# Kernel optimization log

Measured on AMD Instinct MI355X. Metric: run time of the kernel, lower is better.

The kernel has to match this reference:

```python
import jax, jax.numpy as jnp
import numpy as np

DIMS = [14400, 7200, 3600, 1800, 900, 450]  # in_dim then floor(dim/2) per layer
K = 25
BATCH = 256
NSTEPS = 10
OUT_DIM = 2


def setup_inputs() -> dict:
    key = jax.random.key(0)
    ks = jax.random.split(key, 13)
    inp = {"input": jax.random.normal(ks[0], (BATCH, NSTEPS, DIMS[0]), dtype=jnp.float32)}
    w_scale = (2.0 / K) ** 0.5  # matches normal_(0, (2/K)**0.5) init
    for i in range(5):
        d_prev, d = DIMS[i], DIMS[i + 1]
        inp[f"knn{i}"] = jax.random.randint(ks[1 + i], (d, K), 0, d_prev)
        inp[f"w{i}"] = w_scale * jax.random.normal(ks[6 + i], (d, K), dtype=jnp.float32)
        inp[f"b{i}"] = jnp.zeros((1, d), dtype=jnp.float32)
    inp["fc_w"] = jax.random.normal(ks[11], (OUT_DIM, DIMS[-1]), dtype=jnp.float32) * (1.0 / DIMS[-1] ** 0.5)
    inp["fc_b"] = jnp.zeros((OUT_DIM,), dtype=jnp.float32)
    return inp


def reference(input, knn0, knn1, knn2, knn3, knn4,
              w0, w1, w2, w3, w4, b0, b1, b2, b3, b4, fc_w, fc_b):
    # Faithful to the torch module: the synapses/membranes dicts are never
    # reassigned inside the step loop, so every snntorch Synaptic call sees
    # zero state: reset = Heaviside(0 - thr) = 0, syn = alpha*0 + I = I,
    # mem = beta*0 + syn = I.  The returned mem (x) is therefore exactly the
    # layer drive, there is no cross-step recurrence, and `angles` is
    # overwritten each step, so only the final timestep reaches the output.
    knns = (knn0, knn1, knn2, knn3, knn4)
    ws = (w0, w1, w2, w3, w4)
    bs = (b0, b1, b2, b3, b4)
    x = input[:, -1, :]  # [B, in_dim] -- last step (permute(1,0,2) then input[step])
    for knn, w, b in zip(knns, ws, bs):
        # gather KNN inputs [B, dim, K], weight locally, reduce over K, add bias
        x = jnp.einsum('bdk,dk->bd', x[:, knn], w) + b
    angles = x @ fc_w.T + fc_b  # fc_angle
    return angles  # (mem4_rec, spk4_rec are empty lists in the original)
```

## Files before the change

kernel.cpp:

```cpp
#include <hip/hip_runtime.h>

#define NSTEPS 10
#define D_IN   14400
#define BATCH  256
#define KNN_K  25

#define L0D 7200
#define L1D 3600
#define L2D 1800
#define L3D 900
#define L4D 450

#define G0 113
#define G1 57
#define G2 29
#define G3 15
#define G4 8
#define SPG 832
#define O0 0
#define O1 (G0*SPG)
#define O2 (O1 + G1*SPG)
#define O3 (O2 + G2*SPG)
#define O4 (O3 + G3*SPG)
#define OTOT (O4 + G4*SPG)

__device__ __forceinline__ unsigned bf16b(float x) {
    unsigned u = __float_as_uint(x);
    return (u + 0x7fffu + ((u >> 16) & 1u)) >> 16;
}

__device__ __forceinline__ void gpair(unsigned u, const char* actb, float& s0, float& s1) {
    unsigned av = *(const unsigned*)(actb + (u & 0xffffu));
    float wf = __uint_as_float(u & 0xffff0000u);
    s0 = fmaf(__uint_as_float(av << 16),          wf, s0);
    s1 = fmaf(__uint_as_float(av & 0xffff0000u),  wf, s1);
}

__global__ void repack_tiles(const int* __restrict__ k0, const float* __restrict__ w0,
                             const int* __restrict__ k1, const float* __restrict__ w1,
                             const int* __restrict__ k2, const float* __restrict__ w2,
                             const int* __restrict__ k3, const float* __restrict__ w3,
                             const int* __restrict__ k4, const float* __restrict__ w4,
                             uint2* __restrict__ tile)
{
    int s = blockIdx.x * 256 + threadIdx.x;
    if (s >= OTOT) return;
    const int* kp; const float* wp; int dim, t;
    if      (s < O1) { kp = k0; wp = w0; dim = L0D; t = s;      }
    else if (s < O2) { kp = k1; wp = w1; dim = L1D; t = s - O1; }
    else if (s < O3) { kp = k2; wp = w2; dim = L2D; t = s - O2; }
    else if (s < O4) { kp = k3; wp = w3; dim = L3D; t = s - O3; }
    else             { kp = k4; wp = w4; dim = L4D; t = s - O4; }
    int g    = t / SPG;
    int rem  = t - g * SPG;
    int j    = rem >> 6;
    int lane = rem & 63;
    int r    = g * 64 + lane;
    unsigned vx = 0, vy = 0;
    if (r < dim) {
        int e0 = 2 * j, e1 = 2 * j + 1;
        if (e0 < KNN_K) vx = (bf16b(wp[r * KNN_K + e0]) << 16) | ((unsigned)kp[r * KNN_K + e0] << 2);
        if (e1 < KNN_K) vy = (bf16b(wp[r * KNN_K + e1]) << 16) | ((unsigned)kp[r * KNN_K + e1] << 2);
    }
    tile[s] = make_uint2(vx, vy);
}

__global__ __launch_bounds__(512, 4)
void lcn_l0(const float* __restrict__ input, const uint2* __restrict__ tile,
            const float* __restrict__ bias0, unsigned* __restrict__ y0)
{
    __shared__ unsigned act[D_IN];
    const int tid = threadIdx.x;
    const int p   = blockIdx.x & 127;
    const int h   = blockIdx.x >> 7;

    const float4* r0 = (const float4*)(input + ((size_t)(2 * p)     * NSTEPS + (NSTEPS - 1)) * D_IN);
    const float4* r1 = (const float4*)(input + ((size_t)(2 * p + 1) * NSTEPS + (NSTEPS - 1)) * D_IN);
    for (int i = tid; i < D_IN / 4; i += 512) {
        float4 a = r0[i], b = r1[i];
        uint4 wd;
        wd.x = bf16b(a.x) | (bf16b(b.x) << 16);
        wd.y = bf16b(a.y) | (bf16b(b.y) << 16);
        wd.z = bf16b(a.z) | (bf16b(b.z) << 16);
        wd.w = bf16b(a.w) | (bf16b(b.w) << 16);
        *(uint4*)(act + i * 4) = wd;
    }
    __syncthreads();
    const char* actb = (const char*)act;

    const int rbase = h ? 3584 : 0;
    const int rend  = h ? 7200 : 3584;
#pragma unroll
    for (int i = 0; i < 8; ++i) {
        int r = rbase + tid + i * 512;
        if (r < rend) {
            const uint2* tp = tile + (size_t)(r >> 6) * SPG + (r & 63);
            float s0 = bias0[r], s1 = s0;
#pragma unroll
            for (int j = 0; j < 13; ++j) {
                uint2 u = tp[j * 64];
                gpair(u.x, actb, s0, s1);
                gpair(u.y, actb, s0, s1);
            }
            y0[(size_t)p * L0D + r] = bf16b(s0) | (bf16b(s1) << 16);
        }
    }
}

template<int DIM>
__device__ __forceinline__ void k2_layer(unsigned* act, const uint2* tile,
                                         const float* __restrict__ bias, int tid)
{
    constexpr int NI = (DIM + 1023) / 1024;
    float s0[NI], s1[NI];
    const char* actb = (const char*)act;
#pragma unroll
    for (int i = 0; i < NI; ++i) {
        int r = tid + i * 1024;
        if (r < DIM) {
            const uint2* tp = tile + (size_t)(r >> 6) * SPG + (r & 63);
            float a = bias[r], b = a;
#pragma unroll
            for (int j = 0; j < 13; ++j) {
                uint2 u = tp[j * 64];
                gpair(u.x, actb, a, b);
                gpair(u.y, actb, a, b);
            }
            s0[i] = a; s1[i] = b;
        }
    }
    __syncthreads();
#pragma unroll
    for (int i = 0; i < NI; ++i) {
        int r = tid + i * 1024;
        if (r < DIM) act[r] = bf16b(s0[i]) | (bf16b(s1[i]) << 16);
    }
    __syncthreads();
}

__global__ __launch_bounds__(1024, 4)
void lcn_rest(const unsigned* __restrict__ y0, const uint2* __restrict__ tile,
              const float* __restrict__ bias1, const float* __restrict__ bias2,
              const float* __restrict__ bias3, const float* __restrict__ bias4,
              const float* __restrict__ fc_w,  const float* __restrict__ fc_b,
              float* __restrict__ out)
{
    __shared__ unsigned act[L0D];
    const int tid = threadIdx.x;
    const int p   = blockIdx.x;

    const uint4* src = (const uint4*)(y0 + (size_t)p * L0D);
#pragma unroll
    for (int i = 0; i < 2; ++i) {
        int q = tid + i * 1024;
        if (q < L0D / 4) *(uint4*)(act + q * 4) = src[q];
    }
    __syncthreads();

    k2_layer<L1D>(act, tile + O1, bias1, tid);
    k2_layer<L2D>(act, tile + O2, bias2, tid);
    k2_layer<L3D>(act, tile + O3, bias3, tid);
    k2_layer<L4D>(act, tile + O4, bias4, tid);

    const int wv = tid >> 6, lane = tid & 63;
    if (wv < 4) {
        const int j = wv & 1, o = wv >> 1;
        float s = 0.f;
#pragma unroll
        for (int it = 0; it < 8; ++it) {
            int r = lane + it * 64;
            if (r < L4D) {
                unsigned av = act[r];
                float xv = j ? __uint_as_float(av & 0xffff0000u)
                             : __uint_as_float(av << 16);
                s += xv * fc_w[o * L4D + r];
            }
        }
#pragma unroll
        for (int off = 32; off > 0; off >>= 1) s += __shfl_xor(s, off);
        if (lane == 0) out[(2 * p + j) * 2 + o] = s + fc_b[o];
    }
}

extern "C" void kernel_launch(void* const* d_in, const int* in_sizes, int n_in,
                              void* d_out, int out_size, void* d_ws, size_t ws_size,
                              hipStream_t stream) {
    const float* input = (const float*)d_in[0];
    const int*   knn[5];
    const float* w[5];
    const float* bias[5];
    for (int i = 0; i < 5; ++i) {
        knn[i]  = (const int*)  d_in[1 + 3 * i];
        w[i]    = (const float*)d_in[2 + 3 * i];
        bias[i] = (const float*)d_in[3 + 3 * i];
    }
    const float* fc_w = (const float*)d_in[16];
    const float* fc_b = (const float*)d_in[17];
    float* out = (float*)d_out;

    uint2*    tile = (uint2*)d_ws;
    unsigned* y0   = (unsigned*)((char*)d_ws + (size_t)OTOT * 8);

    repack_tiles<<<(OTOT + 255) / 256, 256, 0, stream>>>(
        knn[0], w[0], knn[1], w[1], knn[2], w[2], knn[3], w[3], knn[4], w[4], tile);

    lcn_l0<<<256, 512, 0, stream>>>(input, tile, bias[0], y0);

    lcn_rest<<<128, 1024, 0, stream>>>(y0, tile, bias[1], bias[2], bias[3], bias[4],
                                       fc_w, fc_b, out);
}
```

Baseline: 37.45 us.

## Split layer 1 into its own two-way-split kernel and pre-pack input in prep

Moves the fp32-to-bf16 packing of the last-timestep input into the prep kernel, so layer 0 blocks only copy already-packed pairs into shared memory. Layer 1 is pulled out of the single-block-per-pair tail kernel into a separate kernel with 256 blocks, each computing half the rows, which doubles parallelism for that layer. The layer 0 launch bound changes from 4 to 2 blocks per CU. The cost is an extra kernel launch and extra global round trips for the packed input and the layer-1 output.

```diff
diff --git a/kernel.cpp b/kernel.cpp
--- a/kernel.cpp
+++ b/kernel.cpp
@@ -17,13 +17,15 @@
 #define G3 15
 #define G4 8
 #define SPG 832
-#define O0 0
 #define O1 (G0*SPG)
 #define O2 (O1 + G1*SPG)
 #define O3 (O2 + G2*SPG)
 #define O4 (O3 + G3*SPG)
 #define OTOT (O4 + G4*SPG)
 
+#define NPAIR 128
+#define NPACK (NPAIR * (D_IN/4))
+
 __device__ __forceinline__ unsigned bf16b(float x) {
     unsigned u = __float_as_uint(x);
     return (u + 0x7fffu + ((u >> 16) & 1u)) >> 16;
@@ -36,55 +38,63 @@
     s1 = fmaf(__uint_as_float(av & 0xffff0000u),  wf, s1);
 }
 
-__global__ void repack_tiles(const int* __restrict__ k0, const float* __restrict__ w0,
-                             const int* __restrict__ k1, const float* __restrict__ w1,
-                             const int* __restrict__ k2, const float* __restrict__ w2,
-                             const int* __restrict__ k3, const float* __restrict__ w3,
-                             const int* __restrict__ k4, const float* __restrict__ w4,
-                             uint2* __restrict__ tile)
+__global__ void prep_kernel(const int* __restrict__ k0, const float* __restrict__ w0,
+                            const int* __restrict__ k1, const float* __restrict__ w1,
+                            const int* __restrict__ k2, const float* __restrict__ w2,
+                            const int* __restrict__ k3, const float* __restrict__ w3,
+                            const int* __restrict__ k4, const float* __restrict__ w4,
+                            const float* __restrict__ input,
+                            uint2* __restrict__ tile, uint4* __restrict__ xpk)
 {
     int s = blockIdx.x * 256 + threadIdx.x;
-    if (s >= OTOT) return;
-    const int* kp; const float* wp; int dim, t;
-    if      (s < O1) { kp = k0; wp = w0; dim = L0D; t = s;      }
-    else if (s < O2) { kp = k1; wp = w1; dim = L1D; t = s - O1; }
-    else if (s < O3) { kp = k2; wp = w2; dim = L2D; t = s - O2; }
-    else if (s < O4) { kp = k3; wp = w3; dim = L3D; t = s - O3; }
-    else             { kp = k4; wp = w4; dim = L4D; t = s - O4; }
-    int g    = t / SPG;
-    int rem  = t - g * SPG;
-    int j    = rem >> 6;
-    int lane = rem & 63;
-    int r    = g * 64 + lane;
-    unsigned vx = 0, vy = 0;
-    if (r < dim) {
-        int e0 = 2 * j, e1 = 2 * j + 1;
-        if (e0 < KNN_K) vx = (bf16b(wp[r * KNN_K + e0]) << 16) | ((unsigned)kp[r * KNN_K + e0] << 2);
-        if (e1 < KNN_K) vy = (bf16b(wp[r * KNN_K + e1]) << 16) | ((unsigned)kp[r * KNN_K + e1] << 2);
-    }
-    tile[s] = make_uint2(vx, vy);
-}
-
-__global__ __launch_bounds__(512, 4)
-void lcn_l0(const float* __restrict__ input, const uint2* __restrict__ tile,
-            const float* __restrict__ bias0, unsigned* __restrict__ y0)
-{
-    __shared__ unsigned act[D_IN];
-    const int tid = threadIdx.x;
-    const int p   = blockIdx.x & 127;
-    const int h   = blockIdx.x >> 7;
-
-    const float4* r0 = (const float4*)(input + ((size_t)(2 * p)     * NSTEPS + (NSTEPS - 1)) * D_IN);
-    const float4* r1 = (const float4*)(input + ((size_t)(2 * p + 1) * NSTEPS + (NSTEPS - 1)) * D_IN);
-    for (int i = tid; i < D_IN / 4; i += 512) {
-        float4 a = r0[i], b = r1[i];
+    if (s < OTOT) {
+        const int* kp; const float* wp; int dim, t;
+        if      (s < O1) { kp = k0; wp = w0; dim = L0D; t = s;      }
+        else if (s < O2) { kp = k1; wp = w1; dim = L1D; t = s - O1; }
+        else if (s < O3) { kp = k2; wp = w2; dim = L2D; t = s - O2; }
+        else if (s < O4) { kp = k3; wp = w3; dim = L3D; t = s - O3; }
+        else             { kp = k4; wp = w4; dim = L4D; t = s - O4; }
+        int g    = t / SPG;
+        int rem  = t - g * SPG;
+        int j    = rem >> 6;
+        int lane = rem & 63;
+        int r    = g * 64 + lane;
+        unsigned vx = 0, vy = 0;
+        if (r < dim) {
+            int e0 = 2 * j, e1 = 2 * j + 1;
+            if (e0 < KNN_K) vx = (bf16b(wp[r * KNN_K + e0]) << 16) | ((unsigned)kp[r * KNN_K + e0] << 2);
+            if (e1 < KNN_K) vy = (bf16b(wp[r * KNN_K + e1]) << 16) | ((unsigned)kp[r * KNN_K + e1] << 2);
+        }
+        tile[s] = make_uint2(vx, vy);
+        return;
+    }
+    int t = s - OTOT;
+    if (t < NPACK) {
+        int p = t / (D_IN / 4);
+        int c = t - p * (D_IN / 4);
+        const float4 a = *(const float4*)(input + ((size_t)(2 * p)     * NSTEPS + (NSTEPS - 1)) * D_IN + 4 * c);
+        const float4 b = *(const float4*)(input + ((size_t)(2 * p + 1) * NSTEPS + (NSTEPS - 1)) * D_IN + 4 * c);
         uint4 wd;
         wd.x = bf16b(a.x) | (bf16b(b.x) << 16);
         wd.y = bf16b(a.y) | (bf16b(b.y) << 16);
         wd.z = bf16b(a.z) | (bf16b(b.z) << 16);
         wd.w = bf16b(a.w) | (bf16b(b.w) << 16);
-        *(uint4*)(act + i * 4) = wd;
-    }
+        xpk[(size_t)p * (D_IN / 4) + c] = wd;
+    }
+}
+
+__global__ __launch_bounds__(512, 2)
+void lcn_l0(const uint4* __restrict__ xpk, const uint2* __restrict__ tile,
+            const float* __restrict__ bias0, unsigned* __restrict__ y0)
+{
+    __shared__ unsigned act[D_IN];
+    const int tid = threadIdx.x;
+    const int p   = blockIdx.x & 127;
+    const int h   = blockIdx.x >> 7;
+
+    const uint4* src = xpk + (size_t)p * (D_IN / 4);
+    for (int i = tid; i < D_IN / 4; i += 512)
+        *(uint4*)(act + i * 4) = src[i];
     __syncthreads();
     const char* actb = (const char*)act;
 
@@ -107,6 +117,40 @@
     }
 }
 
+__global__ __launch_bounds__(512, 4)
+void lcn_l1(const unsigned* __restrict__ y0, const uint2* __restrict__ tile,
+            const float* __restrict__ bias1, unsigned* __restrict__ y1)
+{
+    __shared__ unsigned act[L0D];
+    const int tid = threadIdx.x;
+    const int p   = blockIdx.x & 127;
+    const int h   = blockIdx.x >> 7;
+
+    const uint4* src = (const uint4*)(y0 + (size_t)p * L0D);
+    for (int i = tid; i < L0D / 4; i += 512)
+        *(uint4*)(act + i * 4) = src[i];
+    __syncthreads();
+    const char* actb = (const char*)act;
+
+    const int rbase = h ? 1792 : 0;
+    const int rend  = h ? 3600 : 1792;
+#pragma unroll
+    for (int i = 0; i < 4; ++i) {
+        int r = rbase + tid + i * 512;
+        if (r < rend) {
+            const uint2* tp = tile + O1 + (size_t)(r >> 6) * SPG + (r & 63);
+            float s0 = bias1[r], s1 = s0;
+#pragma unroll
+            for (int j = 0; j < 13; ++j) {
+                uint2 u = tp[j * 64];
+                gpair(u.x, actb, s0, s1);
+                gpair(u.y, actb, s0, s1);
+            }
+            y1[(size_t)p * L1D + r] = bf16b(s0) | (bf16b(s1) << 16);
+        }
+    }
+}
+
 template<int DIM>
 __device__ __forceinline__ void k2_layer(unsigned* act, const uint2* tile,
                                          const float* __restrict__ bias, int tid)
@@ -139,25 +183,20 @@
 }
 
 __global__ __launch_bounds__(1024, 4)
-void lcn_rest(const unsigned* __restrict__ y0, const uint2* __restrict__ tile,
-              const float* __restrict__ bias1, const float* __restrict__ bias2,
-              const float* __restrict__ bias3, const float* __restrict__ bias4,
+void lcn_rest(const unsigned* __restrict__ y1, const uint2* __restrict__ tile,
+              const float* __restrict__ bias2, const float* __restrict__ bias3,
+              const float* __restrict__ bias4,
               const float* __restrict__ fc_w,  const float* __restrict__ fc_b,
               float* __restrict__ out)
 {
-    __shared__ unsigned act[L0D];
+    __shared__ unsigned act[L1D];
     const int tid = threadIdx.x;
     const int p   = blockIdx.x;
 
-    const uint4* src = (const uint4*)(y0 + (size_t)p * L0D);
-#pragma unroll
-    for (int i = 0; i < 2; ++i) {
-        int q = tid + i * 1024;
-        if (q < L0D / 4) *(uint4*)(act + q * 4) = src[q];
-    }
-    __syncthreads();
-
-    k2_layer<L1D>(act, tile + O1, bias1, tid);
+    const uint4* src = (const uint4*)(y1 + (size_t)p * L1D);
+    if (tid < L1D / 4) *(uint4*)(act + tid * 4) = src[tid];
+    __syncthreads();
+
     k2_layer<L2D>(act, tile + O2, bias2, tid);
     k2_layer<L3D>(act, tile + O3, bias3, tid);
     k2_layer<L4D>(act, tile + O4, bias4, tid);
@@ -198,14 +237,20 @@
     const float* fc_b = (const float*)d_in[17];
     float* out = (float*)d_out;
 
-    uint2*    tile = (uint2*)d_ws;
-    unsigned* y0   = (unsigned*)((char*)d_ws + (size_t)OTOT * 8);
-
-    repack_tiles<<<(OTOT + 255) / 256, 256, 0, stream>>>(
-        knn[0], w[0], knn[1], w[1], knn[2], w[2], knn[3], w[3], knn[4], w[4], tile);
-
-    lcn_l0<<<256, 512, 0, stream>>>(input, tile, bias[0], y0);
-
-    lcn_rest<<<128, 1024, 0, stream>>>(y0, tile, bias[1], bias[2], bias[3], bias[4],
+    char* base = (char*)d_ws;
+    uint2*    tile = (uint2*)   base;
+    uint4*    xpk  = (uint4*)  (base + (size_t)OTOT * 8);
+    unsigned* y0   = (unsigned*)(base + (size_t)OTOT * 8 + (size_t)NPAIR * D_IN * 4);
+    unsigned* y1   = (unsigned*)(base + (size_t)OTOT * 8 + (size_t)NPAIR * D_IN * 4
+                                      + (size_t)NPAIR * L0D * 4);
+
+    const int nprep = OTOT + NPACK;
+    prep_kernel<<<(nprep + 255) / 256, 256, 0, stream>>>(
+        knn[0], w[0], knn[1], w[1], knn[2], w[2], knn[3], w[3], knn[4], w[4],
+        input, tile, xpk);
+
+    lcn_l0<<<256, 512, 0, stream>>>(xpk, tile, bias[0], y0);
+    lcn_l1<<<256, 512, 0, stream>>>(y0, tile, bias[1], y1);
+    lcn_rest<<<128, 1024, 0, stream>>>(y1, tile, bias[2], bias[3], bias[4],
                                        fc_w, fc_b, out);
 }
```

Result: no change. 37.16 us (-0.8%).

## Pack four batch rows per gather and split layers across more kernels

Applied to the files above, without the earlier changes.

Activations are now packed as four bf16 batch rows per 8-byte LDS word, so each gathered neighbor index feeds four FMAs instead of two. This halves the number of KNN gathers and tile reads per sample. The input bf16 packing moves into the prep kernel alongside the weight repack. Layers 0-2 each become a separate kernel that splits rows four ways across blocks, giving 256 blocks per layer instead of 128 serial blocks for the later layers. The cost is more kernel launches and extra global round trips for the y1 and y2 intermediates, and a 115KB LDS buffer in layer 0 that limits it to one block per CU.

```diff
diff --git a/kernel.cpp b/kernel.cpp
--- a/kernel.cpp
+++ b/kernel.cpp
@@ -2,7 +2,6 @@
 
 #define NSTEPS 10
 #define D_IN   14400
-#define BATCH  256
 #define KNN_K  25
 
 #define L0D 7200
@@ -17,168 +16,222 @@
 #define G3 15
 #define G4 8
 #define SPG 832
-#define O0 0
 #define O1 (G0*SPG)
 #define O2 (O1 + G1*SPG)
 #define O3 (O2 + G2*SPG)
 #define O4 (O3 + G3*SPG)
 #define OTOT (O4 + G4*SPG)
 
+#define NG    64
+#define PACKQ (D_IN/4)
+#define NPACK (NG * PACKQ)
+
 __device__ __forceinline__ unsigned bf16b(float x) {
     unsigned u = __float_as_uint(x);
     return (u + 0x7fffu + ((u >> 16) & 1u)) >> 16;
 }
 
-__device__ __forceinline__ void gpair(unsigned u, const char* actb, float& s0, float& s1) {
-    unsigned av = *(const unsigned*)(actb + (u & 0xffffu));
-    float wf = __uint_as_float(u & 0xffff0000u);
-    s0 = fmaf(__uint_as_float(av << 16),          wf, s0);
-    s1 = fmaf(__uint_as_float(av & 0xffff0000u),  wf, s1);
-}
-
-__global__ void repack_tiles(const int* __restrict__ k0, const float* __restrict__ w0,
-                             const int* __restrict__ k1, const float* __restrict__ w1,
-                             const int* __restrict__ k2, const float* __restrict__ w2,
-                             const int* __restrict__ k3, const float* __restrict__ w3,
-                             const int* __restrict__ k4, const float* __restrict__ w4,
-                             uint2* __restrict__ tile)
+__device__ __forceinline__ void gp4(unsigned u, const char* actb,
+                                    float& a0, float& a1, float& a2, float& a3) {
+    const uint2 av = *(const uint2*)(actb + 8u * (u & 0xffffu));
+    const float wf = __uint_as_float(u & 0xffff0000u);
+    a0 = fmaf(__uint_as_float(av.x << 16),         wf, a0);
+    a1 = fmaf(__uint_as_float(av.x & 0xffff0000u), wf, a1);
+    a2 = fmaf(__uint_as_float(av.y << 16),         wf, a2);
+    a3 = fmaf(__uint_as_float(av.y & 0xffff0000u), wf, a3);
+}
+
+__global__ void prep_kernel(const int* __restrict__ k0, const float* __restrict__ w0,
+                            const int* __restrict__ k1, const float* __restrict__ w1,
+                            const int* __restrict__ k2, const float* __restrict__ w2,
+                            const int* __restrict__ k3, const float* __restrict__ w3,
+                            const int* __restrict__ k4, const float* __restrict__ w4,
+                            const float* __restrict__ input,
+                            uint2* __restrict__ tile, uint2* __restrict__ xpk)
 {
     int s = blockIdx.x * 256 + threadIdx.x;
-    if (s >= OTOT) return;
-    const int* kp; const float* wp; int dim, t;
-    if      (s < O1) { kp = k0; wp = w0; dim = L0D; t = s;      }
-    else if (s < O2) { kp = k1; wp = w1; dim = L1D; t = s - O1; }
-    else if (s < O3) { kp = k2; wp = w2; dim = L2D; t = s - O2; }
-    else if (s < O4) { kp = k3; wp = w3; dim = L3D; t = s - O3; }
-    else             { kp = k4; wp = w4; dim = L4D; t = s - O4; }
-    int g    = t / SPG;
-    int rem  = t - g * SPG;
-    int j    = rem >> 6;
-    int lane = rem & 63;
-    int r    = g * 64 + lane;
-    unsigned vx = 0, vy = 0;
-    if (r < dim) {
-        int e0 = 2 * j, e1 = 2 * j + 1;
-        if (e0 < KNN_K) vx = (bf16b(wp[r * KNN_K + e0]) << 16) | ((unsigned)kp[r * KNN_K + e0] << 2);
-        if (e1 < KNN_K) vy = (bf16b(wp[r * KNN_K + e1]) << 16) | ((unsigned)kp[r * KNN_K + e1] << 2);
-    }
-    tile[s] = make_uint2(vx, vy);
-}
-
-__global__ __launch_bounds__(512, 4)
-void lcn_l0(const float* __restrict__ input, const uint2* __restrict__ tile,
-            const float* __restrict__ bias0, unsigned* __restrict__ y0)
-{
-    __shared__ unsigned act[D_IN];
-    const int tid = threadIdx.x;
-    const int p   = blockIdx.x & 127;
-    const int h   = blockIdx.x >> 7;
-
-    const float4* r0 = (const float4*)(input + ((size_t)(2 * p)     * NSTEPS + (NSTEPS - 1)) * D_IN);
-    const float4* r1 = (const float4*)(input + ((size_t)(2 * p + 1) * NSTEPS + (NSTEPS - 1)) * D_IN);
-    for (int i = tid; i < D_IN / 4; i += 512) {
-        float4 a = r0[i], b = r1[i];
-        uint4 wd;
-        wd.x = bf16b(a.x) | (bf16b(b.x) << 16);
-        wd.y = bf16b(a.y) | (bf16b(b.y) << 16);
-        wd.z = bf16b(a.z) | (bf16b(b.z) << 16);
-        wd.w = bf16b(a.w) | (bf16b(b.w) << 16);
-        *(uint4*)(act + i * 4) = wd;
-    }
+    if (s < OTOT) {
+        const int* kp; const float* wp; int dim, t;
+        if      (s < O1) { kp = k0; wp = w0; dim = L0D; t = s;      }
+        else if (s < O2) { kp = k1; wp = w1; dim = L1D; t = s - O1; }
+        else if (s < O3) { kp = k2; wp = w2; dim = L2D; t = s - O2; }
+        else if (s < O4) { kp = k3; wp = w3; dim = L3D; t = s - O3; }
+        else             { kp = k4; wp = w4; dim = L4D; t = s - O4; }
+        int g    = t / SPG;
+        int rem  = t - g * SPG;
+        int j    = rem >> 6;
+        int lane = rem & 63;
+        int r    = g * 64 + lane;
+        unsigned vx = 0, vy = 0;
+        if (r < dim) {
+            int e0 = 2 * j, e1 = 2 * j + 1;
+            if (e0 < KNN_K) vx = (bf16b(wp[r * KNN_K + e0]) << 16) | (unsigned)kp[r * KNN_K + e0];
+            if (e1 < KNN_K) vy = (bf16b(wp[r * KNN_K + e1]) << 16) | (unsigned)kp[r * KNN_K + e1];
+        }
+        tile[s] = make_uint2(vx, vy);
+        return;
+    }
+    int t = s - OTOT;
+    if (t < NPACK) {
+        int g = t / PACKQ;
+        int c = t - g * PACKQ;
+        float4 r[4];
+#pragma unroll
+        for (int b = 0; b < 4; ++b)
+            r[b] = *(const float4*)(input + ((size_t)(4 * g + b) * NSTEPS + NSTEPS - 1) * D_IN + 4 * c);
+        uint4 lo, hi;
+        lo.x = bf16b(r[0].x) | (bf16b(r[1].x) << 16);
+        lo.y = bf16b(r[2].x) | (bf16b(r[3].x) << 16);
+        lo.z = bf16b(r[0].y) | (bf16b(r[1].y) << 16);
+        lo.w = bf16b(r[2].y) | (bf16b(r[3].y) << 16);
+        hi.x = bf16b(r[0].z) | (bf16b(r[1].z) << 16);
+        hi.y = bf16b(r[2].z) | (bf16b(r[3].z) << 16);
+        hi.z = bf16b(r[0].w) | (bf16b(r[1].w) << 16);
+        hi.w = bf16b(r[2].w) | (bf16b(r[3].w) << 16);
+        uint4* dst = (uint4*)(xpk + ((size_t)g * D_IN + 4 * c));
+        dst[0] = lo;
+        dst[1] = hi;
+    }
+}
+
+template<int PREV, int DIM, int NSPLIT, int BLK>
+__device__ __forceinline__ void glayer(const uint2* __restrict__ xin_g,
+                                       uint2* __restrict__ yout_g,
+                                       const uint2* __restrict__ tile,
+                                       const float* __restrict__ bias,
+                                       uint2* act, int tid, int q)
+{
+    const uint4* src = (const uint4*)xin_g;
+    for (int i = tid; i < PREV / 2; i += BLK)
+        *(uint4*)(act + 2 * i) = src[i];
     __syncthreads();
     const char* actb = (const char*)act;
-
-    const int rbase = h ? 3584 : 0;
-    const int rend  = h ? 7200 : 3584;
-#pragma unroll
-    for (int i = 0; i < 8; ++i) {
-        int r = rbase + tid + i * 512;
-        if (r < rend) {
+    constexpr int ROWS = DIM / NSPLIT;
+    const int r0 = q * ROWS;
+#pragma unroll
+    for (int i = 0; i < (ROWS + BLK - 1) / BLK; ++i) {
+        int rr = tid + i * BLK;
+        if (rr < ROWS) {
+            int r = r0 + rr;
             const uint2* tp = tile + (size_t)(r >> 6) * SPG + (r & 63);
-            float s0 = bias0[r], s1 = s0;
+            const float bv = bias[r];
+            float x0 = bv, x1 = bv, x2 = bv, x3 = bv;
+            float z0 = 0, z1 = 0, z2 = 0, z3 = 0;
 #pragma unroll
             for (int j = 0; j < 13; ++j) {
                 uint2 u = tp[j * 64];
-                gpair(u.x, actb, s0, s1);
-                gpair(u.y, actb, s0, s1);
-            }
-            y0[(size_t)p * L0D + r] = bf16b(s0) | (bf16b(s1) << 16);
-        }
-    }
-}
-
-template<int DIM>
-__device__ __forceinline__ void k2_layer(unsigned* act, const uint2* tile,
-                                         const float* __restrict__ bias, int tid)
-{
-    constexpr int NI = (DIM + 1023) / 1024;
-    float s0[NI], s1[NI];
-    const char* actb = (const char*)act;
-#pragma unroll
-    for (int i = 0; i < NI; ++i) {
-        int r = tid + i * 1024;
-        if (r < DIM) {
-            const uint2* tp = tile + (size_t)(r >> 6) * SPG + (r & 63);
-            float a = bias[r], b = a;
-#pragma unroll
-            for (int j = 0; j < 13; ++j) {
-                uint2 u = tp[j * 64];
-                gpair(u.x, actb, a, b);
-                gpair(u.y, actb, a, b);
-            }
-            s0[i] = a; s1[i] = b;
-        }
-    }
-    __syncthreads();
-#pragma unroll
-    for (int i = 0; i < NI; ++i) {
-        int r = tid + i * 1024;
-        if (r < DIM) act[r] = bf16b(s0[i]) | (bf16b(s1[i]) << 16);
-    }
-    __syncthreads();
-}
-
-__global__ __launch_bounds__(1024, 4)
-void lcn_rest(const unsigned* __restrict__ y0, const uint2* __restrict__ tile,
-              const float* __restrict__ bias1, const float* __restrict__ bias2,
+                gp4(u.x, actb, x0, x1, x2, x3);
+                gp4(u.y, actb, z0, z1, z2, z3);
+            }
+            x0 += z0; x1 += z1; x2 += z2; x3 += z3;
+            yout_g[r] = make_uint2(bf16b(x0) | (bf16b(x1) << 16),
+                                   bf16b(x2) | (bf16b(x3) << 16));
+        }
+    }
+}
+
+__global__ __launch_bounds__(1024, 1)
+void lcn_l0(const uint2* __restrict__ xpk, const uint2* __restrict__ tile,
+            const float* __restrict__ bias0, uint2* __restrict__ y0)
+{
+    __shared__ uint2 act[D_IN];
+    const int g = blockIdx.x >> 2, q = blockIdx.x & 3;
+    glayer<D_IN, L0D, 4, 1024>(xpk + (size_t)g * D_IN, y0 + (size_t)g * L0D,
+                               tile, bias0, act, threadIdx.x, q);
+}
+
+__global__ __launch_bounds__(1024, 2)
+void lcn_l1(const uint2* __restrict__ y0, const uint2* __restrict__ tile,
+            const float* __restrict__ bias1, uint2* __restrict__ y1)
+{
+    __shared__ uint2 act[L0D];
+    const int g = blockIdx.x >> 2, q = blockIdx.x & 3;
+    glayer<L0D, L1D, 4, 1024>(y0 + (size_t)g * L0D, y1 + (size_t)g * L1D,
+                              tile + O1, bias1, act, threadIdx.x, q);
+}
+
+__global__ __launch_bounds__(512, 4)
+void lcn_l2(const uint2* __restrict__ y1, const uint2* __restrict__ tile,
+            const float* __restrict__ bias2, uint2* __restrict__ y2)
+{
+    __shared__ uint2 act[L1D];
+    const int g = blockIdx.x >> 2, q = blockIdx.x & 3;
+    glayer<L1D, L2D, 4, 512>(y1 + (size_t)g * L1D, y2 + (size_t)g * L2D,
+                             tile + O2, bias2, act, threadIdx.x, q);
+}
+
+__global__ __launch_bounds__(1024, 2)
+void lcn_rest(const uint2* __restrict__ y2, const uint2* __restrict__ tile,
               const float* __restrict__ bias3, const float* __restrict__ bias4,
               const float* __restrict__ fc_w,  const float* __restrict__ fc_b,
               float* __restrict__ out)
 {
-    __shared__ unsigned act[L0D];
+    __shared__ uint2 act[L2D + L3D + L4D];
     const int tid = threadIdx.x;
-    const int p   = blockIdx.x;
-
-    const uint4* src = (const uint4*)(y0 + (size_t)p * L0D);
-#pragma unroll
-    for (int i = 0; i < 2; ++i) {
-        int q = tid + i * 1024;
-        if (q < L0D / 4) *(uint4*)(act + q * 4) = src[q];
-    }
-    __syncthreads();
-
-    k2_layer<L1D>(act, tile + O1, bias1, tid);
-    k2_layer<L2D>(act, tile + O2, bias2, tid);
-    k2_layer<L3D>(act, tile + O3, bias3, tid);
-    k2_layer<L4D>(act, tile + O4, bias4, tid);
-
+    const int g   = blockIdx.x;
+
+    const uint4* src = (const uint4*)(y2 + (size_t)g * L2D);
+    if (tid < L2D / 2) *(uint4*)(act + 2 * tid) = src[tid];
+    __syncthreads();
+
+    {
+        const char* actb = (const char*)act;
+        if (tid < L3D) {
+            const int r = tid;
+            const uint2* tp = tile + O3 + (size_t)(r >> 6) * SPG + (r & 63);
+            const float bv = bias3[r];
+            float x0 = bv, x1 = bv, x2 = bv, x3 = bv, z0 = 0, z1 = 0, z2 = 0, z3 = 0;
+#pragma unroll
+            for (int j = 0; j < 13; ++j) {
+                uint2 u = tp[j * 64];
+                gp4(u.x, actb, x0, x1, x2, x3);
+                gp4(u.y, actb, z0, z1, z2, z3);
+            }
+            x0 += z0; x1 += z1; x2 += z2; x3 += z3;
+            act[L2D + r] = make_uint2(bf16b(x0) | (bf16b(x1) << 16),
+                                      bf16b(x2) | (bf16b(x3) << 16));
+        }
+    }
+    __syncthreads();
+
+    {
+        const char* actb = (const char*)(act + L2D);
+        if (tid < L4D) {
+            const int r = tid;
+            const uint2* tp = tile + O4 + (size_t)(r >> 6) * SPG + (r & 63);
+            const float bv = bias4[r];
+            float x0 = bv, x1 = bv, x2 = bv, x3 = bv, z0 = 0, z1 = 0, z2 = 0, z3 = 0;
+#pragma unroll
+            for (int j = 0; j < 13; ++j) {
+                uint2 u = tp[j * 64];
+                gp4(u.x, actb, x0, x1, x2, x3);
+                gp4(u.y, actb, z0, z1, z2, z3);
+            }
+            x0 += z0; x1 += z1; x2 += z2; x3 += z3;
+            act[L2D + L3D + r] = make_uint2(bf16b(x0) | (bf16b(x1) << 16),
+                                            bf16b(x2) | (bf16b(x3) << 16));
+        }
+    }
+    __syncthreads();
+
+    const uint2* C = act + L2D + L3D;
     const int wv = tid >> 6, lane = tid & 63;
-    if (wv < 4) {
-        const int j = wv & 1, o = wv >> 1;
+    if (wv < 8) {
+        const int o = wv >> 2, j = wv & 3;
         float s = 0.f;
 #pragma unroll
         for (int it = 0; it < 8; ++it) {
             int r = lane + it * 64;
             if (r < L4D) {
-                unsigned av = act[r];
-                float xv = j ? __uint_as_float(av & 0xffff0000u)
-                             : __uint_as_float(av << 16);
-                s += xv * fc_w[o * L4D + r];
+                uint2 av = C[r];
+                unsigned wsel = (j >> 1) ? av.y : av.x;
+                unsigned h = (j & 1) ? (wsel & 0xffff0000u) : (wsel << 16);
+                s += __uint_as_float(h) * fc_w[o * L4D + r];
             }
         }
 #pragma unroll
         for (int off = 32; off > 0; off >>= 1) s += __shfl_xor(s, off);
-        if (lane == 0) out[(2 * p + j) * 2 + o] = s + fc_b[o];
+        if (lane == 0) out[(4 * g + j) * 2 + o] = s + fc_b[o];
     }
 }
 
@@ -198,14 +251,20 @@
     const float* fc_b = (const float*)d_in[17];
     float* out = (float*)d_out;
 
-    uint2*    tile = (uint2*)d_ws;
-    unsigned* y0   = (unsigned*)((char*)d_ws + (size_t)OTOT * 8);
-
-    repack_tiles<<<(OTOT + 255) / 256, 256, 0, stream>>>(
-        knn[0], w[0], knn[1], w[1], knn[2], w[2], knn[3], w[3], knn[4], w[4], tile);
-
-    lcn_l0<<<256, 512, 0, stream>>>(input, tile, bias[0], y0);
-
-    lcn_rest<<<128, 1024, 0, stream>>>(y0, tile, bias[1], bias[2], bias[3], bias[4],
-                                       fc_w, fc_b, out);
-}
+    char* base = (char*)d_ws;
+    uint2* tile = (uint2*)base;
+    uint2* xpk  = (uint2*)(base + (size_t)OTOT * 8);
+    uint2* y0   = (uint2*)((char*)xpk + (size_t)NG * D_IN * 8);
+    uint2* y1   = (uint2*)((char*)y0  + (size_t)NG * L0D * 8);
+    uint2* y2   = (uint2*)((char*)y1  + (size_t)NG * L1D * 8);
+
+    const int nprep = OTOT + NPACK;
+    prep_kernel<<<(nprep + 255) / 256, 256, 0, stream>>>(
+        knn[0], w[0], knn[1], w[1], knn[2], w[2], knn[3], w[3], knn[4], w[4],
+        input, tile, xpk);
+
+    lcn_l0<<<NG * 4, 1024, 0, stream>>>(xpk, tile, bias[0], y0);
+    lcn_l1<<<NG * 4, 1024, 0, stream>>>(y0, tile, bias[1], y1);
+    lcn_l2<<<NG * 4, 512, 0, stream>>>(y1, tile, bias[2], y2);
+    lcn_rest<<<NG, 1024, 0, stream>>>(y2, tile, bias[3], bias[4], fc_w, fc_b, out);
+}
```

Result: slower. 40.93 us (+9.3%).

## Bank-sorted KNN tile layout, prepacked input, split accumulators, double-buffered tail

Applied to the files above, without the earlier changes.

The repack kernel now sorts each row's 25 neighbours by LDS bank and rotates the slots by lane, to reduce LDS bank conflicts in the gather loops. Converting the last-timestep input to bf16 pairs moves into the prep kernel, which writes a packed buffer that lcn_l0 copies into shared memory. The gather loops use two independent accumulator pairs to shorten FMA dependency chains. The tail kernel ping-pongs between two shared buffers, which removes one barrier per layer. In exchange, it adds an extra global round trip for the packed input and more per-thread sorting work in prep.

```diff
diff --git a/kernel.cpp b/kernel.cpp
--- a/kernel.cpp
+++ b/kernel.cpp
@@ -2,7 +2,6 @@
 
 #define NSTEPS 10
 #define D_IN   14400
-#define BATCH  256
 #define KNN_K  25
 
 #define L0D 7200
@@ -10,6 +9,7 @@
 #define L2D 1800
 #define L3D 900
 #define L4D 450
+#define NROWS 13950
 
 #define G0 113
 #define G1 57
@@ -17,163 +17,181 @@
 #define G3 15
 #define G4 8
 #define SPG 832
-#define O0 0
 #define O1 (G0*SPG)
 #define O2 (O1 + G1*SPG)
 #define O3 (O2 + G2*SPG)
 #define O4 (O3 + G3*SPG)
 #define OTOT (O4 + G4*SPG)
 
+#define NPAIR 128
+#define NPACK (NPAIR * (D_IN/4))
+
+#define SPLIT0 3584
+
 __device__ __forceinline__ unsigned bf16b(float x) {
     unsigned u = __float_as_uint(x);
     return (u + 0x7fffu + ((u >> 16) & 1u)) >> 16;
 }
 
-__device__ __forceinline__ void gpair(unsigned u, const char* actb, float& s0, float& s1) {
+__device__ __forceinline__ void gpairB(unsigned u, const char* __restrict__ actb,
+                                       float& s0, float& s1) {
     unsigned av = *(const unsigned*)(actb + (u & 0xffffu));
     float wf = __uint_as_float(u & 0xffff0000u);
     s0 = fmaf(__uint_as_float(av << 16),          wf, s0);
     s1 = fmaf(__uint_as_float(av & 0xffff0000u),  wf, s1);
 }
 
-__global__ void repack_tiles(const int* __restrict__ k0, const float* __restrict__ w0,
-                             const int* __restrict__ k1, const float* __restrict__ w1,
-                             const int* __restrict__ k2, const float* __restrict__ w2,
-                             const int* __restrict__ k3, const float* __restrict__ w3,
-                             const int* __restrict__ k4, const float* __restrict__ w4,
-                             uint2* __restrict__ tile)
-{
-    int s = blockIdx.x * 256 + threadIdx.x;
-    if (s >= OTOT) return;
-    const int* kp; const float* wp; int dim, t;
-    if      (s < O1) { kp = k0; wp = w0; dim = L0D; t = s;      }
-    else if (s < O2) { kp = k1; wp = w1; dim = L1D; t = s - O1; }
-    else if (s < O3) { kp = k2; wp = w2; dim = L2D; t = s - O2; }
-    else if (s < O4) { kp = k3; wp = w3; dim = L3D; t = s - O3; }
-    else             { kp = k4; wp = w4; dim = L4D; t = s - O4; }
-    int g    = t / SPG;
-    int rem  = t - g * SPG;
-    int j    = rem >> 6;
-    int lane = rem & 63;
-    int r    = g * 64 + lane;
-    unsigned vx = 0, vy = 0;
-    if (r < dim) {
-        int e0 = 2 * j, e1 = 2 * j + 1;
-        if (e0 < KNN_K) vx = (bf16b(wp[r * KNN_K + e0]) << 16) | ((unsigned)kp[r * KNN_K + e0] << 2);
-        if (e1 < KNN_K) vy = (bf16b(wp[r * KNN_K + e1]) << 16) | ((unsigned)kp[r * KNN_K + e1] << 2);
-    }
-    tile[s] = make_uint2(vx, vy);
-}
-
-__global__ __launch_bounds__(512, 4)
-void lcn_l0(const float* __restrict__ input, const uint2* __restrict__ tile,
-            const float* __restrict__ bias0, unsigned* __restrict__ y0)
-{
-    __shared__ unsigned act[D_IN];
-    const int tid = threadIdx.x;
-    const int p   = blockIdx.x & 127;
-    const int h   = blockIdx.x >> 7;
-
-    const float4* r0 = (const float4*)(input + ((size_t)(2 * p)     * NSTEPS + (NSTEPS - 1)) * D_IN);
-    const float4* r1 = (const float4*)(input + ((size_t)(2 * p + 1) * NSTEPS + (NSTEPS - 1)) * D_IN);
-    for (int i = tid; i < D_IN / 4; i += 512) {
-        float4 a = r0[i], b = r1[i];
+__global__ void prep_kernel(const int* __restrict__ k0, const float* __restrict__ w0,
+                            const int* __restrict__ k1, const float* __restrict__ w1,
+                            const int* __restrict__ k2, const float* __restrict__ w2,
+                            const int* __restrict__ k3, const float* __restrict__ w3,
+                            const int* __restrict__ k4, const float* __restrict__ w4,
+                            const float* __restrict__ input,
+                            uint2* __restrict__ tile, uint4* __restrict__ xpk)
+{
+    const int s = blockIdx.x * 256 + threadIdx.x;
+    if (s < NROWS) {
+        const int* kp; const float* wp; int dl, obase;
+        if      (s < L0D)             { kp = k0; wp = w0; dl = s;         obase = 0;  }
+        else if (s < L0D+L1D)         { kp = k1; wp = w1; dl = s - L0D;   obase = O1; }
+        else if (s < L0D+L1D+L2D)     { kp = k2; wp = w2; dl = s-L0D-L1D; obase = O2; }
+        else if (s < L0D+L1D+L2D+L3D) { kp = k3; wp = w3; dl = s-L0D-L1D-L2D; obase = O3; }
+        else                          { kp = k4; wp = w4; dl = s-L0D-L1D-L2D-L3D; obase = O4; }
+        const int g = dl >> 6, l = dl & 63;
+
+        int   idx[KNN_K]; float wv[KNN_K]; int bk[KNN_K];
+#pragma unroll
+        for (int k = 0; k < KNN_K; ++k) {
+            idx[k] = kp[dl * KNN_K + k];
+            wv[k]  = wp[dl * KNN_K + k];
+            bk[k]  = idx[k] & 31;
+        }
+        const int lm = l - (l >= 50 ? 50 : (l >= 25 ? 25 : 0));
+        unsigned* tw = (unsigned*)tile + 2u * (unsigned)(obase + g * SPG);
+#pragma unroll
+        for (int k = 0; k < KNN_K; ++k) {
+            int rank = 0;
+#pragma unroll
+            for (int j = 0; j < KNN_K; ++j)
+                rank += (bk[j] < bk[k]) || (bk[j] == bk[k] && j < k);
+            int slot = rank + lm; if (slot >= KNN_K) slot -= KNN_K;
+            unsigned u = (bf16b(wv[k]) << 16) | ((unsigned)idx[k] << 2);
+            tw[((slot >> 1) * 64 + l) * 2 + (slot & 1)] = u;
+        }
+        tw[(12 * 64 + l) * 2 + 1] = 0;
+        return;
+    }
+    const int t = s - NROWS;
+    if (t < NPACK) {
+        const int p = t / (D_IN / 4);
+        const int c = t - p * (D_IN / 4);
+        const float4 a = *(const float4*)(input + ((size_t)(2*p)   * NSTEPS + NSTEPS-1) * D_IN + 4*c);
+        const float4 b = *(const float4*)(input + ((size_t)(2*p+1) * NSTEPS + NSTEPS-1) * D_IN + 4*c);
         uint4 wd;
         wd.x = bf16b(a.x) | (bf16b(b.x) << 16);
         wd.y = bf16b(a.y) | (bf16b(b.y) << 16);
         wd.z = bf16b(a.z) | (bf16b(b.z) << 16);
         wd.w = bf16b(a.w) | (bf16b(b.w) << 16);
-        *(uint4*)(act + i * 4) = wd;
-    }
+        xpk[(size_t)p * (D_IN / 4) + c] = wd;
+    }
+}
+
+__global__ __launch_bounds__(512, 2)
+void lcn_l0(const uint4* __restrict__ xpk, const uint2* __restrict__ tile,
+            const float* __restrict__ bias0, unsigned* __restrict__ y0)
+{
+    __shared__ unsigned act[D_IN];
+    const int tid = threadIdx.x;
+    const int p   = blockIdx.x & 127;
+    const int h   = blockIdx.x >> 7;
+
+    const uint4* src = xpk + (size_t)p * (D_IN / 4);
+    for (int i = tid; i < D_IN / 4; i += 512)
+        *(uint4*)(act + i * 4) = src[i];
     __syncthreads();
     const char* actb = (const char*)act;
 
-    const int rbase = h ? 3584 : 0;
-    const int rend  = h ? 7200 : 3584;
+    const int rbase = h ? SPLIT0 : 0;
+    const int rend  = h ? L0D    : SPLIT0;
 #pragma unroll
     for (int i = 0; i < 8; ++i) {
         int r = rbase + tid + i * 512;
         if (r < rend) {
             const uint2* tp = tile + (size_t)(r >> 6) * SPG + (r & 63);
-            float s0 = bias0[r], s1 = s0;
+            float a = bias0[r], b = a, c = 0.f, d = 0.f;
 #pragma unroll
             for (int j = 0; j < 13; ++j) {
                 uint2 u = tp[j * 64];
-                gpair(u.x, actb, s0, s1);
-                gpair(u.y, actb, s0, s1);
+                gpairB(u.x, actb, a, b);
+                gpairB(u.y, actb, c, d);
             }
-            y0[(size_t)p * L0D + r] = bf16b(s0) | (bf16b(s1) << 16);
+            a += c; b += d;
+            y0[(size_t)p * L0D + r] = bf16b(a) | (bf16b(b) << 16);
         }
     }
 }
 
 template<int DIM>
-__device__ __forceinline__ void k2_layer(unsigned* act, const uint2* tile,
-                                         const float* __restrict__ bias, int tid)
-{
-    constexpr int NI = (DIM + 1023) / 1024;
-    float s0[NI], s1[NI];
-    const char* actb = (const char*)act;
-#pragma unroll
-    for (int i = 0; i < NI; ++i) {
+__device__ __forceinline__ void glayerT(const char* __restrict__ actb,
+                                        unsigned* __restrict__ yout,
+                                        const uint2* __restrict__ tb,
+                                        const float* __restrict__ bias, int tid)
+{
+#pragma unroll
+    for (int i = 0; i < (DIM + 1023) / 1024; ++i) {
         int r = tid + i * 1024;
         if (r < DIM) {
-            const uint2* tp = tile + (size_t)(r >> 6) * SPG + (r & 63);
-            float a = bias[r], b = a;
+            const uint2* tp = tb + (size_t)(r >> 6) * SPG + (r & 63);
+            float a = bias[r], b = a, c = 0.f, d = 0.f;
 #pragma unroll
             for (int j = 0; j < 13; ++j) {
                 uint2 u = tp[j * 64];
-                gpair(u.x, actb, a, b);
-                gpair(u.y, actb, a, b);
+                gpairB(u.x, actb, a, b);
+                gpairB(u.y, actb, c, d);
             }
-            s0[i] = a; s1[i] = b;
-        }
-    }
-    __syncthreads();
-#pragma unroll
-    for (int i = 0; i < NI; ++i) {
-        int r = tid + i * 1024;
-        if (r < DIM) act[r] = bf16b(s0[i]) | (bf16b(s1[i]) << 16);
-    }
-    __syncthreads();
-}
-
-__global__ __launch_bounds__(1024, 4)
-void lcn_rest(const unsigned* __restrict__ y0, const uint2* __restrict__ tile,
-              const float* __restrict__ bias1, const float* __restrict__ bias2,
-              const float* __restrict__ bias3, const float* __restrict__ bias4,
-              const float* __restrict__ fc_w,  const float* __restrict__ fc_b,
+            a += c; b += d;
+            yout[r] = bf16b(a) | (bf16b(b) << 16);
+        }
+    }
+}
+
+__global__ __launch_bounds__(1024)
+void lcn_tail(const unsigned* __restrict__ y0, const uint2* __restrict__ tile,
+              const float* __restrict__ b1, const float* __restrict__ b2,
+              const float* __restrict__ b3, const float* __restrict__ b4,
+              const float* __restrict__ fc_w, const float* __restrict__ fc_b,
               float* __restrict__ out)
 {
-    __shared__ unsigned act[L0D];
+    __shared__ unsigned sm[L0D + L1D];
     const int tid = threadIdx.x;
     const int p   = blockIdx.x;
 
     const uint4* src = (const uint4*)(y0 + (size_t)p * L0D);
-#pragma unroll
-    for (int i = 0; i < 2; ++i) {
-        int q = tid + i * 1024;
-        if (q < L0D / 4) *(uint4*)(act + q * 4) = src[q];
-    }
-    __syncthreads();
-
-    k2_layer<L1D>(act, tile + O1, bias1, tid);
-    k2_layer<L2D>(act, tile + O2, bias2, tid);
-    k2_layer<L3D>(act, tile + O3, bias3, tid);
-    k2_layer<L4D>(act, tile + O4, bias4, tid);
-
-    const int wv = tid >> 6, lane = tid & 63;
-    if (wv < 4) {
-        const int j = wv & 1, o = wv >> 1;
+    for (int i = tid; i < L0D / 4; i += 1024)
+        *(uint4*)(sm + 4 * i) = src[i];
+    __syncthreads();
+
+    glayerT<L1D>((const char*)sm,         sm + L0D,        tile + O1, b1, tid);
+    __syncthreads();
+    glayerT<L2D>((const char*)(sm + L0D), sm,              tile + O2, b2, tid);
+    __syncthreads();
+    glayerT<L3D>((const char*)sm,         sm + L2D,        tile + O3, b3, tid);
+    __syncthreads();
+    glayerT<L4D>((const char*)(sm + L2D), sm + L2D + L3D,  tile + O4, b4, tid);
+    __syncthreads();
+
+    const unsigned* C = sm + L2D + L3D;
+    if (tid < 256) {
+        const int wv = tid >> 6, lane = tid & 63;
+        const int o = wv >> 1, j = wv & 1;
         float s = 0.f;
 #pragma unroll
         for (int it = 0; it < 8; ++it) {
             int r = lane + it * 64;
             if (r < L4D) {
-                unsigned av = act[r];
-                float xv = j ? __uint_as_float(av & 0xffff0000u)
-                             : __uint_as_float(av << 16);
-                s += xv * fc_w[o * L4D + r];
+                unsigned av = C[r];
+                unsigned hbits = j ? (av & 0xffff0000u) : (av << 16);
+                s += __uint_as_float(hbits) * fc_w[o * L4D + r];
             }
         }
 #pragma unroll
@@ -198,14 +216,18 @@
     const float* fc_b = (const float*)d_in[17];
     float* out = (float*)d_out;
 
-    uint2*    tile = (uint2*)d_ws;
-    unsigned* y0   = (unsigned*)((char*)d_ws + (size_t)OTOT * 8);
-
-    repack_tiles<<<(OTOT + 255) / 256, 256, 0, stream>>>(
-        knn[0], w[0], knn[1], w[1], knn[2], w[2], knn[3], w[3], knn[4], w[4], tile);
-
-    lcn_l0<<<256, 512, 0, stream>>>(input, tile, bias[0], y0);
-
-    lcn_rest<<<128, 1024, 0, stream>>>(y0, tile, bias[1], bias[2], bias[3], bias[4],
-                                       fc_w, fc_b, out);
-}
+    char* base = (char*)d_ws;
+    uint2*    tile = (uint2*)base;
+    uint4*    xpk  = (uint4*)(base + (size_t)OTOT * 8);
+    unsigned* y0   = (unsigned*)((char*)xpk + (size_t)NPAIR * D_IN * 4);
+
+    const int nprep = NROWS + NPACK;
+    prep_kernel<<<(nprep + 255) / 256, 256, 0, stream>>>(
+        knn[0], w[0], knn[1], w[1], knn[2], w[2], knn[3], w[3], knn[4], w[4],
+        input, tile, xpk);
+
+    lcn_l0<<<256, 512, 0, stream>>>(xpk, tile, bias[0], y0);
+
+    lcn_tail<<<NPAIR, 1024, 0, stream>>>(y0, tile, bias[1], bias[2], bias[3], bias[4],
+                                         fc_w, fc_b, out);
+}
```

After: 40.77 us. 1.09x slower.
